# Kernel tuning notes

Hardware: AMD Instinct MI355X
Metric: run time of the kernel (lower is better)

Reference implementation:

```python
import jax, jax.numpy as jnp
import numpy as np

EPS = 1e-7
B, N, DIM, NH, HD, WIN, HASH_WIN = 2, 1024, 512, 8, 64, 64, 8


def expmap0(v, c):
    sqrt_c = jnp.clip(jnp.sqrt(c), EPS)
    v_norm = jnp.linalg.norm(v, axis=-1, keepdims=True)
    is_zero = v_norm < EPS
    safe = jnp.clip(v_norm, EPS)
    mag = jnp.tanh(sqrt_c * safe) / sqrt_c
    return jnp.where(is_zero, jnp.zeros_like(v), mag * (v / safe))


def poincare_dist(x, y, c):
    # x: (B,H,N,1,D), y: (B,H,N,W,D), c: (B,1,1,1,1) -> (B,H,N,W)
    sqrt_c = jnp.clip(jnp.sqrt(c), EPS)
    x2 = jnp.sum(x * x, -1, keepdims=True)
    y2 = jnp.sum(y * y, -1, keepdims=True)
    xy = jnp.sum(x * y, -1, keepdims=True)
    num = (1 - 2 * c * xy + c * y2) * x + (1 - c * x2) * (-y)
    den = 1 - 2 * c * xy + c * c * x2 * y2
    diff = num / jnp.clip(den, EPS)
    dn = jnp.linalg.norm(diff, axis=-1)
    arg = jnp.minimum(jnp.squeeze(sqrt_c, -1) * jnp.clip(dn, EPS), 1.0 - EPS)
    return 2.0 * jnp.arctanh(arg) / jnp.squeeze(sqrt_c, -1)


def sliding_windows(t, w):
    # t: (B,H,N,D) -> (B,H,N,w,D), left-padded causal window
    Bb, H, Nn, D = t.shape
    pad = jnp.zeros((Bb, H, w - 1, D), t.dtype)
    tp = jnp.concatenate([pad, t], axis=2)
    idx = jnp.arange(w)[None, :] + jnp.arange(Nn)[:, None]  # (N,w)
    return tp[:, :, idx, :]


def layernorm(x, s, b):
    m = jnp.mean(x, -1, keepdims=True)
    v = jnp.var(x, -1, keepdims=True)
    return (x - m) / jnp.sqrt(v + 1e-6) * s + b


def rope(x, cos, sin):
    # x: (B,N,H,hd), cos/sin: (N, hd//2) -- complex rotation in real arithmetic
    xr, xi = jnp.split(x, 2, axis=-1)
    cos = cos[None, :, None, :]
    sin = sin[None, :, None, :]
    return jnp.concatenate([xr * cos - xi * sin, xr * sin + xi * cos], axis=-1)


def setup_inputs() -> dict:
    key = jax.random.key(0)
    ks = jax.random.split(key, 10)
    x = jax.random.normal(ks[0], (B, N, DIM), jnp.float32)
    pos = jnp.arange(N, dtype=jnp.float32)
    inv = 1.0 / (10000.0 ** (jnp.arange(0, HD, 2, dtype=jnp.float32) / HD))
    ang = pos[:, None] * inv[None, :]  # (N, HD//2)
    freqs_cos, freqs_sin = jnp.cos(ang), jnp.sin(ang)
    c = jax.random.uniform(ks[1], (B,), jnp.float32) * 0.9 + 0.1
    s = 0.02
    Wq = jax.random.normal(ks[2], (DIM, DIM), jnp.float32) * s
    Wk = jax.random.normal(ks[3], (DIM, DIM), jnp.float32) * s
    Wv = jax.random.normal(ks[4], (DIM, DIM), jnp.float32) * s
    Wo = jax.random.normal(ks[5], (DIM, DIM), jnp.float32) * s
    W1 = jax.random.normal(ks[6], (DIM, 4 * DIM), jnp.float32) * s
    W2 = jax.random.normal(ks[7], (4 * DIM, DIM), jnp.float32) * s
    bq = jnp.zeros((DIM,)); bk = jnp.zeros((DIM,)); bv = jnp.zeros((DIM,))
    bo = jnp.zeros((DIM,)); b1 = jnp.zeros((4 * DIM,)); b2 = jnp.zeros((DIM,))
    ln1_s = jnp.ones((DIM,)); ln1_b = jnp.zeros((DIM,))
    ln2_s = jnp.ones((DIM,)); ln2_b = jnp.zeros((DIM,))
    geo_scale = jnp.ones((NH, 1, 1), jnp.float32)
    hash_offset = jax.random.normal(ks[8], (1, 1, NH, HD), jnp.float32) * 0.01
    return dict(x=x, freqs_cos=freqs_cos, freqs_sin=freqs_sin, c=c,
                Wq=Wq, bq=bq, Wk=Wk, bk=bk, Wv=Wv, bv=bv, Wo=Wo, bo=bo,
                W1=W1, b1=b1, W2=W2, b2=b2,
                ln1_s=ln1_s, ln1_b=ln1_b, ln2_s=ln2_s, ln2_b=ln2_b,
                geo_scale=geo_scale, hash_offset=hash_offset)


def reference(x, freqs_cos, freqs_sin, c, Wq, bq, Wk, bk, Wv, bv, Wo, bo,
              W1, b1, W2, b2, ln1_s, ln1_b, ln2_s, ln2_b, geo_scale, hash_offset):
    x_res = x
    xn = layernorm(x, ln1_s, ln1_b)
    q = (xn @ Wq + bq).reshape(B, N, NH, HD)
    k = (xn @ Wk + bk).reshape(B, N, NH, HD)
    v = (xn @ Wv + bv).reshape(B, N, NH, HD)
    q = q + hash_offset * jnp.log(1.0 + HASH_WIN)
    q_rot = rope(q, freqs_cos, freqs_sin)
    k_rot = rope(k, freqs_cos, freqs_sin)
    c_b = c.reshape(B, 1, 1, 1)
    q_h = expmap0(q_rot, c_b)
    k_h = expmap0(k_rot, c_b)
    q_h, k_h, v = (t.transpose(0, 2, 1, 3) for t in (q_h, k_h, v))  # (B,H,N,D)
    k_win = sliding_windows(k_h, WIN)  # (B,H,N,W,D)
    v_win = sliding_windows(v, WIN)
    dist = poincare_dist(q_h[:, :, :, None, :], k_win, c.reshape(B, 1, 1, 1, 1))  # (B,H,N,W)
    scores = -geo_scale * dist
    w = jax.nn.softmax(scores, axis=-1)
    attn = jnp.einsum('bhnw,bhnwd->bhnd', w, v_win)
    attn = attn.transpose(0, 2, 1, 3).reshape(B, N, DIM)
    x_out = x_res + (attn @ Wo + bo)
    h = layernorm(x_out, ln2_s, ln2_b)
    ffn = jax.nn.gelu(h @ W1 + b1) @ W2 + b2
    return x_out + ffn
```

## Files before the change

kernel.cpp:

```cpp
#include <hip/hip_runtime.h>
#include <math.h>
#include <stdint.h>

#define Bn   2
#define Nn   1024
#define DIMn 512
#define NHn  8
#define HDn  64
#define QKVS 1536
#define EPSF 1e-7f

typedef __attribute__((ext_vector_type(8))) short short8;
typedef __attribute__((ext_vector_type(4))) float floatx4;

__device__ __forceinline__ unsigned short f2bf(float f) {
  union { float f; uint32_t u; } v; v.f = f;
  uint32_t u = v.u;
  return (unsigned short)((u + 0x7FFFu + ((u >> 16) & 1u)) >> 16);
}
__device__ __forceinline__ float bf2f(unsigned short h) {
  union { uint32_t u; float f; } v; v.u = ((uint32_t)h) << 16;
  return v.f;
}

__device__ __forceinline__ float wsum(float v) {
#pragma unroll
  for (int m = 32; m >= 1; m >>= 1) v += __shfl_xor(v, m, 64);
  return v;
}
__device__ __forceinline__ float wmax(float v) {
#pragma unroll
  for (int m = 32; m >= 1; m >>= 1) v = fmaxf(v, __shfl_xor(v, m, 64));
  return v;
}

__device__ __forceinline__ float gelu_tanh(float x) {
  const float k0 = 0.7978845608028654f;
  float x3 = x * x * x;
  return 0.5f * x * (1.f + tanhf(k0 * (x + 0.044715f * x3)));
}

__device__ __forceinline__ void glds16(const unsigned short* g, unsigned short* l) {
  __builtin_amdgcn_global_load_lds((const __attribute__((address_space(1))) void*)g,
                                   (__attribute__((address_space(3))) void*)l, 16, 0, 0);
}

__global__ __launch_bounds__(256) void convT_all(
    const float* __restrict__ Wq, const float* __restrict__ Wk,
    const float* __restrict__ Wv, const float* __restrict__ Wo,
    const float* __restrict__ W1, const float* __restrict__ W2,
    unsigned short* __restrict__ Wcat_hi, unsigned short* __restrict__ Wcat_lo,
    unsigned short* __restrict__ Wo_t, unsigned short* __restrict__ W1_t,
    unsigned short* __restrict__ W2_t,
    const float* __restrict__ bq, const float* __restrict__ bk,
    const float* __restrict__ bv, float* __restrict__ bias_cat) {
  __shared__ float t[32][33];
  int bid = blockIdx.x;
  int tid = threadIdx.x;
  if (bid >= 3072) {
    for (int i = tid; i < 512; i += 256) {
      bias_cat[i] = bq[i];
      bias_cat[512 + i] = bk[i];
      bias_cat[1024 + i] = bv[i];
    }
    return;
  }
  const float* W;
  unsigned short* hi;
  unsigned short* lo = nullptr;
  int K, N, tix;
  if (bid < 256)       { W = Wq; hi = Wcat_hi;               lo = Wcat_lo;               K = 512;  N = 512;  tix = bid; }
  else if (bid < 512)  { W = Wk; hi = Wcat_hi + 512 * 512;   lo = Wcat_lo + 512 * 512;   K = 512;  N = 512;  tix = bid - 256; }
  else if (bid < 768)  { W = Wv; hi = Wcat_hi + 1024 * 512;  K = 512;  N = 512;  tix = bid - 512; }
  else if (bid < 1024) { W = Wo; hi = Wo_t;                  K = 512;  N = 512;  tix = bid - 768; }
  else if (bid < 2048) { W = W1; hi = W1_t;                  K = 512;  N = 2048; tix = bid - 1024; }
  else                 { W = W2; hi = W2_t;                  K = 2048; N = 512;  tix = bid - 2048; }
  int ntn = N >> 5;
  int kt = tix / ntn, nt = tix - kt * ntn;
  int k0 = kt * 32, n0 = nt * 32;
  for (int i = tid; i < 1024; i += 256) {
    int r = i >> 5, c = i & 31;
    t[r][c] = W[(size_t)(k0 + r) * N + n0 + c];
  }
  __syncthreads();
  for (int i = tid; i < 1024; i += 256) {
    int r = i >> 5, c = i & 31;
    float v = t[c][r];
    unsigned short h = f2bf(v);
    size_t oi = (size_t)(n0 + r) * K + k0 + c;
    hi[oi] = h;
    if (lo) lo[oi] = f2bf(v - bf2f(h));
  }
}

template <int SPLIT>
__global__ __launch_bounds__(256) void ln_kernel(const float* __restrict__ x,
                                                 const float* __restrict__ g,
                                                 const float* __restrict__ be,
                                                 unsigned short* __restrict__ yhi,
                                                 unsigned short* __restrict__ ylo) {
  __shared__ float red[2][4];
  int row = blockIdx.x;
  int tid = threadIdx.x;
  const float* xr = x + (size_t)row * DIMn;
  float2 xv = *(const float2*)(xr + tid * 2);
  float s  = xv.x + xv.y;
  float s2 = xv.x * xv.x + xv.y * xv.y;
  s = wsum(s); s2 = wsum(s2);
  int wv = tid >> 6;
  if ((tid & 63) == 0) { red[0][wv] = s; red[1][wv] = s2; }
  __syncthreads();
  s  = red[0][0] + red[0][1] + red[0][2] + red[0][3];
  s2 = red[1][0] + red[1][1] + red[1][2] + red[1][3];
  float mean = s * (1.f / DIMn);
  float var  = s2 * (1.f / DIMn) - mean * mean;
  float rstd = rsqrtf(var + 1e-6f);
  int d = tid * 2;
  float2 gv = *(const float2*)(g + d);
  float2 bv = *(const float2*)(be + d);
  float o0 = (xv.x - mean) * rstd * gv.x + bv.x;
  float o1 = (xv.y - mean) * rstd * gv.y + bv.y;
  size_t idx = (size_t)row * DIMn + d;
  unsigned short h0 = f2bf(o0), h1 = f2bf(o1);
  ushort2 hv; hv.x = h0; hv.y = h1;
  *(ushort2*)(yhi + idx) = hv;
  if (SPLIT) {
    ushort2 lv; lv.x = f2bf(o0 - bf2f(h0)); lv.y = f2bf(o1 - bf2f(h1));
    *(ushort2*)(ylo + idx) = lv;
  }
}

template <int BM, int BN, int BKT, int SPLIT, int EPI, int OUTBF16>
__global__ __launch_bounds__(256) void gemm_mfma(
    const unsigned short* __restrict__ Ahi, const unsigned short* __restrict__ Alo,
    const unsigned short* __restrict__ Bhi, const unsigned short* __restrict__ Blo,
    const float* __restrict__ bias, const float* __restrict__ res,
    void* __restrict__ outp, int M, int N, int K) {
  constexpr int FI = BM / 32, FJ = BN / 32;
  constexpr int AE = BM * BKT, BE = BN * BKT;
  constexpr int NB = (SPLIT > 0) ? 2 : 1;
  constexpr int CPR = BKT / 8;
  constexpr int ACH = BM * CPR, BCH = BN * CPR;
  __shared__ unsigned short smem[NB * (AE + BE)];
  unsigned short* AsHi = smem;
  unsigned short* AsLo = smem + ((SPLIT > 0) ? AE : 0);
  unsigned short* BsHi = smem + NB * AE;
  unsigned short* BsLo = BsHi + ((SPLIT > 0) ? BE : 0);

  int tid = threadIdx.x;
  int lane = tid & 63;
  int wid = tid >> 6;
  int wm = (wid >> 1) * (BM / 2), wn = (wid & 1) * (BN / 2);
  int bm = blockIdx.y * BM, bn = blockIdx.x * BN;
  int m16 = lane & 15, kg = lane >> 4;
  bool dos = (SPLIT == 1) || (SPLIT == 2 && bn < 1024);

  floatx4 acc[FI][FJ];
#pragma unroll
  for (int i = 0; i < FI; ++i)
#pragma unroll
    for (int j = 0; j < FJ; ++j) { floatx4 z = {0.f, 0.f, 0.f, 0.f}; acc[i][j] = z; }

  const unsigned short* aph = Ahi + (size_t)bm * K;
  const unsigned short* bph = Bhi + (size_t)bn * K;
  const unsigned short* apl = (SPLIT > 0) ? (Alo + (size_t)bm * K) : nullptr;
  const unsigned short* bpl = (SPLIT > 0) ? (Blo + (size_t)bn * K) : nullptr;

  for (int k0 = 0; k0 < K; k0 += BKT) {
#pragma unroll
    for (int c = tid; c < ACH; c += 256) {
      int row = c / CPR, kk = (c % CPR) * 8;
      glds16(aph + (size_t)row * K + k0 + kk, AsHi + c * 8);
      if (SPLIT > 0 && dos) glds16(apl + (size_t)row * K + k0 + kk, AsLo + c * 8);
    }
#pragma unroll
    for (int c = tid; c < BCH; c += 256) {
      int row = c / CPR, kk = (c % CPR) * 8;
      glds16(bph + (size_t)row * K + k0 + kk, BsHi + c * 8);
      if (SPLIT > 0 && dos) glds16(bpl + (size_t)row * K + k0 + kk, BsLo + c * 8);
    }
    __syncthreads();

#pragma unroll
    for (int ks = 0; ks < BKT / 32; ++ks) {
      short8 ah[FI], bh[FJ];
      short8 al[(SPLIT > 0) ? FI : 1], bl[(SPLIT > 0) ? FJ : 1];
#pragma unroll
      for (int i = 0; i < FI; ++i) {
        int r = wm + i * 16 + m16;
        ah[i] = *(const short8*)&AsHi[r * BKT + ks * 32 + kg * 8];
        if (SPLIT > 0 && dos) al[i] = *(const short8*)&AsLo[r * BKT + ks * 32 + kg * 8];
      }
#pragma unroll
      for (int j = 0; j < FJ; ++j) {
        int r = wn + j * 16 + m16;
        bh[j] = *(const short8*)&BsHi[r * BKT + ks * 32 + kg * 8];
        if (SPLIT > 0 && dos) bl[j] = *(const short8*)&BsLo[r * BKT + ks * 32 + kg * 8];
      }
#pragma unroll
      for (int i = 0; i < FI; ++i)
#pragma unroll
        for (int j = 0; j < FJ; ++j) {
          acc[i][j] = __builtin_amdgcn_mfma_f32_16x16x32_bf16(ah[i], bh[j], acc[i][j], 0, 0, 0);
          if (SPLIT > 0) {
            if (dos) {
              acc[i][j] = __builtin_amdgcn_mfma_f32_16x16x32_bf16(al[i], bh[j], acc[i][j], 0, 0, 0);
              acc[i][j] = __builtin_amdgcn_mfma_f32_16x16x32_bf16(ah[i], bl[j], acc[i][j], 0, 0, 0);
            }
          }
        }
    }
    __syncthreads();
  }

#pragma unroll
  for (int i = 0; i < FI; ++i) {
    int gr0 = bm + wm + i * 16 + kg * 4;
#pragma unroll
    for (int j = 0; j < FJ; ++j) {
      int gc = bn + wn + j * 16 + m16;
      float bsv = bias[gc];
#pragma unroll
      for (int r = 0; r < 4; ++r) {
        size_t idx = (size_t)(gr0 + r) * N + gc;
        float v = acc[i][j][r] + bsv;
        if constexpr (EPI == 1) v += res[idx];
        if constexpr (EPI == 2) v = gelu_tanh(v);
        if constexpr (OUTBF16) ((unsigned short*)outp)[idx] = f2bf(v);
        else ((float*)outp)[idx] = v;
      }
    }
  }
}

__global__ __launch_bounds__(256) void attn_fused(const float* __restrict__ qkv,
                                                  const float* __restrict__ fcos,
                                                  const float* __restrict__ fsin,
                                                  const float* __restrict__ cvec,
                                                  const float* __restrict__ geo,
                                                  const float* __restrict__ hash,
                                                  unsigned short* __restrict__ attn_out) {
  __shared__ unsigned short Qhi[32][64], Qlo[32][64];
  __shared__ unsigned short Khi[96][64], Klo[96][64];
  __shared__ unsigned short Vs[96][72];
  __shared__ float Sf[32][97];
  __shared__ float x2s[32], y2s[96];

  int tid = threadIdx.x, lane = tid & 63, wv = tid >> 6;
  int bid = blockIdx.x;
  int nt = bid & 31, h = (bid >> 5) & 7, b = bid >> 8;
  int n0 = nt * 32;
  float c = cvec[b];
  float sqc = sqrtf(c);
  float gs = geo[h];
  int dr = lane & 31;
  bool hih = lane >= 32;
  const float LOG9 = 2.1972245773362196f;
  float hofr = hash[h * HDn + dr] * LOG9;
  float hofi = hash[h * HDn + dr + 32] * LOG9;

#pragma unroll
  for (int i = 0; i < 8; ++i) {
    int q = wv * 8 + i;
    int n = n0 + q;
    size_t bas = (size_t)(b * Nn + n) * QKVS + h * HDn;
    float qr = qkv[bas + dr] + hofr;
    float qi = qkv[bas + dr + 32] + hofi;
    float cs = fcos[n * 32 + dr], sn = fsin[n * 32 + dr];
    float qv = hih ? (qr * sn + qi * cs) : (qr * cs - qi * sn);
    float nq = sqrtf(wsum(qv * qv));
    float sq = fmaxf(nq, EPSF);
    float mag = tanhf(sqc * sq) / sqc;
    float oq = (nq < EPSF) ? 0.f : mag * (qv / sq);
    unsigned short hh = f2bf(oq);
    Qhi[q][lane] = hh;
    Qlo[q][lane] = f2bf(oq - bf2f(hh));
    if (lane == 0) x2s[q] = (nq < EPSF) ? 0.f : mag * mag;
  }
#pragma unroll 4
  for (int i = 0; i < 24; ++i) {
    int r = wv * 24 + i;
    int gi = n0 - 64 + r;
    float ok = 0.f, vf = 0.f, y2 = 0.f;
    if (gi >= 0) {
      size_t bas = (size_t)(b * Nn + gi) * QKVS + h * HDn;
      float kr = qkv[bas + 512 + dr];
      float ki = qkv[bas + 512 + dr + 32];
      vf = qkv[bas + 1024 + lane];
      float cs = fcos[gi * 32 + dr], sn = fsin[gi * 32 + dr];
      float kv = hih ? (kr * sn + ki * cs) : (kr * cs - ki * sn);
      float nk = sqrtf(wsum(kv * kv));
      float sk = fmaxf(nk, EPSF);
      float mag = tanhf(sqc * sk) / sqc;
      ok = (nk < EPSF) ? 0.f : mag * (kv / sk);
      y2 = (nk < EPSF) ? 0.f : mag * mag;
    }
    unsigned short hh = f2bf(ok);
    Khi[r][lane] = hh;
    Klo[r][lane] = f2bf(ok - bf2f(hh));
    Vs[r][lane] = f2bf(vf);
    if (lane == 0) y2s[r] = y2;
  }
  __syncthreads();

  int m16 = lane & 15, kg = lane >> 4;
  int mt = wv >> 1;
#pragma unroll
  for (int j = 0; j < 3; ++j) {
    int ntile = (wv & 1) * 3 + j;
    floatx4 acc = {0.f, 0.f, 0.f, 0.f};
#pragma unroll
    for (int ks = 0; ks < 2; ++ks) {
      short8 ah = *(const short8*)&Qhi[mt * 16 + m16][ks * 32 + kg * 8];
      short8 al = *(const short8*)&Qlo[mt * 16 + m16][ks * 32 + kg * 8];
      short8 bh = *(const short8*)&Khi[ntile * 16 + m16][ks * 32 + kg * 8];
      short8 bl = *(const short8*)&Klo[ntile * 16 + m16][ks * 32 + kg * 8];
      acc = __builtin_amdgcn_mfma_f32_16x16x32_bf16(ah, bh, acc, 0, 0, 0);
      acc = __builtin_amdgcn_mfma_f32_16x16x32_bf16(al, bh, acc, 0, 0, 0);
      acc = __builtin_amdgcn_mfma_f32_16x16x32_bf16(ah, bl, acc, 0, 0, 0);
    }
#pragma unroll
    for (int r = 0; r < 4; ++r) Sf[mt * 16 + kg * 4 + r][ntile * 16 + m16] = acc[r];
  }
  __syncthreads();

  for (int i = 0; i < 8; ++i) {
    int nl = wv * 8 + i;
    int r = nl + 1 + lane;
    float xy = Sf[nl][r];
    float x2 = x2s[nl];
    float y2 = y2s[r];

    double cd = c, xyd = xy, y2d = y2, x2d = x2;
    double alpha = 1.0 - 2.0 * cd * xyd + cd * y2d;
    double beta  = 1.0 - cd * x2d;
    double den = 1.0 - 2.0 * cd * xyd + cd * cd * x2d * y2d;
    den = den > 1e-7 ? den : 1e-7;
    double dn2 = alpha * alpha * x2d - 2.0 * alpha * beta * xyd + beta * beta * y2d;
    dn2 = dn2 > 0.0 ? dn2 : 0.0;
    double dn = sqrt(dn2) / den;
    dn = dn > 1e-7 ? dn : 1e-7;
    double arg = (double)sqc * dn;
    if (arg > 0.9999999) arg = 0.9999999;
    double dist = log((1.0 + arg) / (1.0 - arg)) / (double)sqc;
    float sc = (float)(-(double)gs * dist);

    float mx = wmax(sc);
    float e = expf(sc - mx);
    float se = wsum(e);
    Sf[nl][r] = e / se;
  }

  int q4 = lane >> 4, dx = (lane & 15) * 4;
#pragma unroll
  for (int qq = 0; qq < 8; qq += 4) {
    int nl = wv * 8 + qq + q4;
    float a0 = 0.f, a1 = 0.f, a2 = 0.f, a3 = 0.f;
#pragma unroll 8
    for (int j = 0; j < 64; ++j) {
      float w = Sf[nl][nl + 1 + j];
      ushort4 vv = *(const ushort4*)&Vs[nl + 1 + j][dx];
      a0 = fmaf(w, bf2f(vv.x), a0);
      a1 = fmaf(w, bf2f(vv.y), a1);
      a2 = fmaf(w, bf2f(vv.z), a2);
      a3 = fmaf(w, bf2f(vv.w), a3);
    }
    size_t o = (size_t)(b * Nn + n0 + nl) * DIMn + h * HDn + dx;
    ushort4 ov;
    ov.x = f2bf(a0); ov.y = f2bf(a1); ov.z = f2bf(a2); ov.w = f2bf(a3);
    *(ushort4*)&attn_out[o] = ov;
  }
}

extern "C" void kernel_launch(void* const* d_in, const int* in_sizes, int n_in,
                              void* d_out, int out_size, void* d_ws, size_t ws_size,
                              hipStream_t stream) {
  const float* x    = (const float*)d_in[0];
  const float* fcos = (const float*)d_in[1];
  const float* fsin = (const float*)d_in[2];
  const float* cvec = (const float*)d_in[3];
  const float* Wq = (const float*)d_in[4];  const float* bq = (const float*)d_in[5];
  const float* Wk = (const float*)d_in[6];  const float* bk = (const float*)d_in[7];
  const float* Wv = (const float*)d_in[8];  const float* bv = (const float*)d_in[9];
  const float* Wo = (const float*)d_in[10]; const float* bo = (const float*)d_in[11];
  const float* W1 = (const float*)d_in[12]; const float* b1 = (const float*)d_in[13];
  const float* W2 = (const float*)d_in[14]; const float* b2 = (const float*)d_in[15];
  const float* ln1s = (const float*)d_in[16]; const float* ln1b = (const float*)d_in[17];
  const float* ln2s = (const float*)d_in[18]; const float* ln2b = (const float*)d_in[19];
  const float* geo  = (const float*)d_in[20]; const float* hash = (const float*)d_in[21];
  float* out = (float*)d_out;
  char* base = (char*)d_ws;

  unsigned short* Wcat_hi = (unsigned short*)(base + 0);
  unsigned short* Wcat_lo = (unsigned short*)(base + 1572864);
  unsigned short* Wo_t    = (unsigned short*)(base + 3145728);
  unsigned short* W1_t    = (unsigned short*)(base + 3670016);
  unsigned short* W2_t    = (unsigned short*)(base + 5767168);
  unsigned short* xn_hi   = (unsigned short*)(base + 7864320);
  unsigned short* xn_lo   = (unsigned short*)(base + 9961472);
  float*          qkv     = (float*)(base + 12058624);
  unsigned short* attnb   = (unsigned short*)(base + 7864320);
  float*          xout    = (float*)(base + 9961472);
  unsigned short* hbuf    = (unsigned short*)(base + 14155776);
  unsigned short* mid     = (unsigned short*)(base + 16252928);
  float*          bias_cat= (float*)(base + 24641536);

  const int M = Bn * Nn;

  convT_all<<<3073, 256, 0, stream>>>(Wq, Wk, Wv, Wo, W1, W2, Wcat_hi, Wcat_lo,
                                      Wo_t, W1_t, W2_t, bq, bk, bv, bias_cat);
  ln_kernel<1><<<M, 256, 0, stream>>>(x, ln1s, ln1b, xn_hi, xn_lo);
  gemm_mfma<64, 64, 32, 2, 0, 0><<<dim3(QKVS / 64, M / 64), 256, 0, stream>>>(
      xn_hi, xn_lo, Wcat_hi, Wcat_lo, bias_cat, nullptr, qkv, M, QKVS, 512);
  attn_fused<<<Bn * NHn * (Nn / 32), 256, 0, stream>>>(qkv, fcos, fsin, cvec, geo, hash, attnb);
  gemm_mfma<32, 64, 64, 0, 1, 0><<<dim3(DIMn / 64, M / 32), 256, 0, stream>>>(
      attnb, nullptr, Wo_t, nullptr, bo, x, xout, M, DIMn, 512);
  ln_kernel<0><<<M, 256, 0, stream>>>(xout, ln2s, ln2b, hbuf, nullptr);
  gemm_mfma<64, 128, 64, 0, 2, 1><<<dim3(2048 / 128, M / 64), 256, 0, stream>>>(
      hbuf, nullptr, W1_t, nullptr, b1, nullptr, mid, M, 2048, 512);
  gemm_mfma<32, 64, 64, 0, 1, 0><<<dim3(DIMn / 64, M / 32), 256, 0, stream>>>(
      mid, nullptr, W2_t, nullptr, b2, xout, out, M, DIMn, 2048);
}
```

Baseline: 213.7 us.

## Rewrite Poincare distance in float via sech identity and use MFMA for P·V

Replaces the per-score double-precision Poincare distance and arctanh with a single-precision closed form. It precomputes sech² of each query and key norm and takes one log of a ratio, which avoids slow FP64 math and a division. The weighted sum over V moves from scalar FMA loops to bf16 MFMA: attention probabilities go into a zero-padded bf16 tile, V is stored transposed, and LDS rows are padded to reduce bank conflicts. This adds an extra barrier and more LDS use, and rounds the probabilities to bf16, which risks accuracy on the distances and weights.

```diff
diff --git a/kernel.cpp b/kernel.cpp
--- a/kernel.cpp
+++ b/kernel.cpp
@@ -240,11 +240,12 @@
                                                   const float* __restrict__ geo,
                                                   const float* __restrict__ hash,
                                                   unsigned short* __restrict__ attn_out) {
-  __shared__ unsigned short Qhi[32][64], Qlo[32][64];
-  __shared__ unsigned short Khi[96][64], Klo[96][64];
-  __shared__ unsigned short Vs[96][72];
+  __shared__ unsigned short Qhi[32][72], Qlo[32][72];
+  __shared__ unsigned short Khi[96][72], Klo[96][72];
+  __shared__ unsigned short Vt[64][104];
+  __shared__ unsigned short Pb[32][104];
   __shared__ float Sf[32][97];
-  __shared__ float x2s[32], y2s[96];
+  __shared__ float x2s[32], bxs[32], y2s[96], gys[96];
 
   int tid = threadIdx.x, lane = tid & 63, wv = tid >> 6;
   int bid = blockIdx.x;
@@ -252,12 +253,15 @@
   int n0 = nt * 32;
   float c = cvec[b];
   float sqc = sqrtf(c);
+  float rsqc = 1.f / sqc;
   float gs = geo[h];
   int dr = lane & 31;
   bool hih = lane >= 32;
   const float LOG9 = 2.1972245773362196f;
   float hofr = hash[h * HDn + dr] * LOG9;
   float hofi = hash[h * HDn + dr + 32] * LOG9;
+
+  for (int i = tid; i < 32 * 52; i += 256) ((uint32_t*)Pb)[i] = 0u;
 
 #pragma unroll
   for (int i = 0; i < 8; ++i) {
@@ -270,18 +274,25 @@
     float qv = hih ? (qr * sn + qi * cs) : (qr * cs - qi * sn);
     float nq = sqrtf(wsum(qv * qv));
     float sq = fmaxf(nq, EPSF);
-    float mag = tanhf(sqc * sq) / sqc;
+    float t = sqc * sq;
+    float em = expf(-2.f * t);
+    float opem = 1.f + em;
+    float mag = ((1.f - em) / opem) * rsqc;
+    float sech2 = 4.f * em / (opem * opem);
     float oq = (nq < EPSF) ? 0.f : mag * (qv / sq);
     unsigned short hh = f2bf(oq);
     Qhi[q][lane] = hh;
     Qlo[q][lane] = f2bf(oq - bf2f(hh));
-    if (lane == 0) x2s[q] = (nq < EPSF) ? 0.f : mag * mag;
+    if (lane == 0) {
+      x2s[q] = (nq < EPSF) ? 0.f : mag * mag;
+      bxs[q] = (nq < EPSF) ? 1.f : sech2;
+    }
   }
 #pragma unroll 4
   for (int i = 0; i < 24; ++i) {
     int r = wv * 24 + i;
     int gi = n0 - 64 + r;
-    float ok = 0.f, vf = 0.f, y2 = 0.f;
+    float ok = 0.f, vf = 0.f, y2 = 0.f, gy = 1.f;
     if (gi >= 0) {
       size_t bas = (size_t)(b * Nn + gi) * QKVS + h * HDn;
       float kr = qkv[bas + 512 + dr];
@@ -291,15 +302,20 @@
       float kv = hih ? (kr * sn + ki * cs) : (kr * cs - ki * sn);
       float nk = sqrtf(wsum(kv * kv));
       float sk = fmaxf(nk, EPSF);
-      float mag = tanhf(sqc * sk) / sqc;
+      float t = sqc * sk;
+      float em = expf(-2.f * t);
+      float opem = 1.f + em;
+      float mag = ((1.f - em) / opem) * rsqc;
+      float sech2 = 4.f * em / (opem * opem);
       ok = (nk < EPSF) ? 0.f : mag * (kv / sk);
       y2 = (nk < EPSF) ? 0.f : mag * mag;
+      gy = (nk < EPSF) ? 1.f : sech2;
     }
     unsigned short hh = f2bf(ok);
     Khi[r][lane] = hh;
     Klo[r][lane] = f2bf(ok - bf2f(hh));
-    Vs[r][lane] = f2bf(vf);
-    if (lane == 0) y2s[r] = y2;
+    Vt[lane][r] = f2bf(vf);
+    if (lane == 0) { y2s[r] = y2; gys[r] = gy; }
   }
   __syncthreads();
 
@@ -328,47 +344,42 @@
     int nl = wv * 8 + i;
     int r = nl + 1 + lane;
     float xy = Sf[nl][r];
-    float x2 = x2s[nl];
-    float y2 = y2s[r];
-
-    double cd = c, xyd = xy, y2d = y2, x2d = x2;
-    double alpha = 1.0 - 2.0 * cd * xyd + cd * y2d;
-    double beta  = 1.0 - cd * x2d;
-    double den = 1.0 - 2.0 * cd * xyd + cd * cd * x2d * y2d;
-    den = den > 1e-7 ? den : 1e-7;
-    double dn2 = alpha * alpha * x2d - 2.0 * alpha * beta * xyd + beta * beta * y2d;
-    dn2 = dn2 > 0.0 ? dn2 : 0.0;
-    double dn = sqrt(dn2) / den;
-    dn = dn > 1e-7 ? dn : 1e-7;
-    double arg = (double)sqc * dn;
-    if (arg > 0.9999999) arg = 0.9999999;
-    double dist = log((1.0 + arg) / (1.0 - arg)) / (double)sqc;
-    float sc = (float)(-(double)gs * dist);
+    float x2 = x2s[nl], y2 = y2s[r];
+    float bx = bxs[nl], gy = gys[r];
+
+    float den = fmaf(c * c * x2, y2, fmaf(-2.f * c, xy, 1.f));
+    den = fmaxf(den, EPSF);
+    float rden = 1.f / den;
+    float s2 = fmaxf(x2 - 2.f * xy + y2, 0.f);
+    float z = sqrtf(c * s2 * rden);
+    float omz2 = bx * gy * rden;
+    float opz = 1.f + fminf(z, 1.f);
+    float ratio = fminf(opz * opz / omz2, 1.9999999e7f);
+    float sc = -gs * logf(ratio) * rsqc;
 
     float mx = wmax(sc);
     float e = expf(sc - mx);
     float se = wsum(e);
-    Sf[nl][r] = e / se;
-  }
-
-  int q4 = lane >> 4, dx = (lane & 15) * 4;
-#pragma unroll
-  for (int qq = 0; qq < 8; qq += 4) {
-    int nl = wv * 8 + qq + q4;
-    float a0 = 0.f, a1 = 0.f, a2 = 0.f, a3 = 0.f;
-#pragma unroll 8
-    for (int j = 0; j < 64; ++j) {
-      float w = Sf[nl][nl + 1 + j];
-      ushort4 vv = *(const ushort4*)&Vs[nl + 1 + j][dx];
-      a0 = fmaf(w, bf2f(vv.x), a0);
-      a1 = fmaf(w, bf2f(vv.y), a1);
-      a2 = fmaf(w, bf2f(vv.z), a2);
-      a3 = fmaf(w, bf2f(vv.w), a3);
-    }
-    size_t o = (size_t)(b * Nn + n0 + nl) * DIMn + h * HDn + dx;
-    ushort4 ov;
-    ov.x = f2bf(a0); ov.y = f2bf(a1); ov.z = f2bf(a2); ov.w = f2bf(a3);
-    *(ushort4*)&attn_out[o] = ov;
+    Pb[nl][r] = f2bf(e / se);
+  }
+  __syncthreads();
+
+#pragma unroll
+  for (int nt2 = 0; nt2 < 2; ++nt2) {
+    int ntile = (wv & 1) * 2 + nt2;
+    floatx4 acc = {0.f, 0.f, 0.f, 0.f};
+#pragma unroll
+    for (int ks = 0; ks < 3; ++ks) {
+      short8 a = *(const short8*)&Pb[mt * 16 + m16][ks * 32 + kg * 8];
+      short8 bb = *(const short8*)&Vt[ntile * 16 + m16][ks * 32 + kg * 8];
+      acc = __builtin_amdgcn_mfma_f32_16x16x32_bf16(a, bb, acc, 0, 0, 0);
+    }
+#pragma unroll
+    for (int r = 0; r < 4; ++r) {
+      int qrow = mt * 16 + kg * 4 + r;
+      int d = ntile * 16 + m16;
+      attn_out[(size_t)(b * Nn + n0 + qrow) * DIMn + h * HDn + d] = f2bf(acc[r]);
+    }
   }
 }
 
```

Result: faster. 209.0 us (-2.2%).
